# Performance work log

Measured on AMD Instinct MI355X. Metric: run time of the kernel, lower is better.

## Reference

```python
import jax, jax.numpy as jnp
import numpy as np

B, S, V, E, HL = 64, 30, 5000, 300, 256
TWOH = 2 * HL
KB, MAPD, MEMD, MLP, NCLS = 512, 512, 512, 1024, 32
L, T, NMOD, NOPS = 8, 9, 9, 6
IH, IW, CIN = 15, 10, 512 + 128


def setup_inputs():
    key = jax.random.key(0)
    ks = iter(jax.random.split(key, 64))
    g = lambda shape, s=0.05: jax.random.normal(next(ks), shape, jnp.float32) * s
    inp = {}
    inp['image'] = g((B, CIN, IH, IW), 1.0)
    inp['ques'] = jax.random.randint(next(ks), (B, S), 0, V)
    ql = jnp.sort(jax.random.randint(next(ks), (B,), 1, S + 1))[::-1]
    inp['q_len'] = ql.at[0].set(S)
    inp['embed_W'] = g((V, E))
    for d in ('f', 'b'):
        inp['lstm_Wi_' + d] = g((E, 4 * HL))
        inp['lstm_Wh_' + d] = g((HL, 4 * HL))
        inp['lstm_b_' + d] = jnp.zeros((4 * HL,), jnp.float32)
    inp['W1'] = g((T, TWOH, TWOH))
    inp['b_1'] = jnp.zeros((TWOH,), jnp.float32)
    inp['W2_w'] = g((2 * TWOH, TWOH)); inp['W2_b'] = jnp.zeros((TWOH,), jnp.float32)
    inp['W3'] = g((TWOH,))
    inp['c_0'] = g((TWOH,), 1.0)
    inp['Wmod'] = g((TWOH, NMOD))
    inp['ic1_w'] = g((KB, CIN)); inp['ic1_b'] = g((KB,), 1.0)
    inp['ic2_w'] = g((KB, KB)); inp['ic2_b'] = g((KB,), 1.0)
    inp['i2m_w'] = g((MAPD, KB)); inp['i2m_b'] = g((MAPD,), 1.0)
    inp['t2m_w'] = g((TWOH, MAPD)); inp['t2m_b'] = jnp.zeros((MAPD,), jnp.float32)
    inp['cell3_ow'] = g((4, NOPS), 1.0)
    inp['cell3_cw'] = g((4, MAPD)); inp['cell3_cb'] = jnp.zeros((4,), jnp.float32)
    inp['cell4_ow'] = g((2, NOPS), 1.0)
    inp['cell4_cw'] = g((2, MAPD)); inp['cell4_cb'] = jnp.zeros((2,), jnp.float32)
    inp['ans_ow'] = g((2, NOPS), 1.0)
    inp['ans_W'] = g((2, 2 * MAPD, MEMD)); inp['ans_b'] = jnp.zeros((2, MEMD), jnp.float32)
    inp['out1_w'] = g((TWOH + MEMD, MLP)); inp['out1_b'] = jnp.zeros((MLP,), jnp.float32)
    inp['out2_w'] = g((MLP, NCLS)); inp['out2_b'] = jnp.zeros((NCLS,), jnp.float32)
    return inp


def _conv1x1(x, w, b):
    return jnp.einsum('bchw,oc->bohw', x, w) + b[None, :, None, None]


def _lstm_dir(xW, Wh, mask, reverse):
    # xW: [S,B,4H], mask: [S,B,1] ; torch LSTM gate order i,f,g,o
    Bn, Hn = xW.shape[1], Wh.shape[0]
    def step(carry, inp):
        h, c = carry
        xw, m = inp
        z = xw + h @ Wh
        i, f, gg, o = jnp.split(z, 4, axis=-1)
        cn = jax.nn.sigmoid(f) * c + jax.nn.sigmoid(i) * jnp.tanh(gg)
        hn = jax.nn.sigmoid(o) * jnp.tanh(cn)
        return (jnp.where(m, hn, h), jnp.where(m, cn, c)), jnp.where(m, hn, 0.0)
    init = (jnp.zeros((Bn, Hn), xW.dtype), jnp.zeros((Bn, Hn), xW.dtype))
    (hF, _), outs = jax.lax.scan(step, init, (xW, mask), reverse=reverse)
    return hF, outs


def _mix3(ow, x, a, t):
    # soft op mixing (DARTS-style) for 3-input cells: x [B,D,H,W], a [B,H,W], t [B,D]
    w = jax.nn.softmax(ow)
    a4 = a[:, None]; t4 = t[:, :, None, None]
    ops = (x * t4, x + t4, x * a4, x * t4 * a4, x, a4 * t4)
    return jax.nn.elu(sum(w[k] * ops[k] for k in range(NOPS)))


def _mix4(ow, x, a1, a2, t):
    w = jax.nn.softmax(ow)
    a14 = a1[:, None]; a24 = a2[:, None]; t4 = t[:, :, None, None]
    ops = (x * t4, x + t4, x * a14, x * a24, x * a14 * a24, x * t4 * (a14 + a24))
    return jax.nn.elu(sum(w[k] * ops[k] for k in range(NOPS)))


def _forward(image, ques, q_len, embed_W, lstm_Wi_f, lstm_Wh_f, lstm_b_f, lstm_Wi_b, lstm_Wh_b, lstm_b_b, W1, b_1, W2_w, W2_b, W3, c_0, Wmod, ic1_w, ic1_b, ic2_w, ic2_b, i2m_w, i2m_b, t2m_w, t2m_b, cell3_ow, cell3_cw, cell3_cb, cell4_ow, cell4_cw, cell4_cb, ans_ow, ans_W, ans_b, out1_w, out1_b, out2_w, out2_b):
    # img_conv (1x1 conv -> ELU -> 1x1 conv)
    x = jax.nn.elu(_conv1x1(image, ic1_w, ic1_b))
    x = _conv1x1(x, ic2_w, ic2_b)
    Bn, _, Hh, Ww = x.shape
    Sn = ques.shape[1]
    # bi-LSTM over the (packed, i.e. masked) question
    emb = embed_W[ques]                                   # [B,S,E]
    mask = (jnp.arange(Sn)[None, :] < q_len[:, None])     # [B,S]
    mT = mask.T[:, :, None].astype(x.dtype) > 0           # [S,B,1] bool
    xWf = (emb @ lstm_Wi_f + lstm_b_f).transpose(1, 0, 2)
    xWb = (emb @ lstm_Wi_b + lstm_b_b).transpose(1, 0, 2)
    hF, oF = _lstm_dir(xWf, lstm_Wh_f, mT, False)
    hB, oB = _lstm_dir(xWb, lstm_Wh_b, mT, True)
    lstm_out = jnp.concatenate([oF, oB], -1).transpose(1, 0, 2)  # [B,S,2H], zero at pads
    q = jnp.concatenate([hF, hB], -1)                            # [B,2H]
    img_map = _conv1x1(x, i2m_w, i2m_b)                          # [B,MAP,H,W]
    stack = jnp.zeros((Bn, Hh, Ww, L), x.dtype)
    p = jnp.zeros((Bn, L), x.dtype).at[:, 0].set(1.0)
    mem = jnp.zeros((Bn, MEMD), x.dtype)
    c_prev = jnp.tile(c_0[None], (Bn, 1))
    e0 = jnp.zeros((L,), x.dtype).at[0].set(1.0)
    imp_loss = jnp.float32(0.0)
    read = lambda st, pp: jnp.einsum('bhwl,bl->bhw', st, pp)
    dec = lambda pp: jnp.concatenate([pp[:, 1:], jnp.zeros_like(pp[:, :1])], 1) + pp * e0
    for t in range(T):
        u = jnp.concatenate([q @ W1[t] + b_1, c_prev], 1) @ W2_w + W2_b  # [B,2H]
        wl = u @ Wmod                                                     # [B,9]
        ls = jax.nn.log_softmax(wl, axis=1)
        imp_loss = imp_loss - jnp.sum(jnp.exp(ls) * ls)
        w = jnp.exp(ls)
        attn = jax.nn.softmax(jnp.einsum('bsh,h->bs', lstm_out * u[:, None, :], W3), axis=1)
        c = jnp.einsum('bs,bsh->bh', attn, lstm_out)
        c_prev = c
        tmap = c @ t2m_w + t2m_b
        stacks, ps = [], []
        a_top = read(stack, p)     # attention at stack top
        # modules 0-3: overwrite at current pointer (pointer shift is commented out in source)
        for m in range(4):
            out = jnp.einsum('bdhw,d->bhw', _mix3(cell3_ow[m], img_map, a_top, tmap), cell3_cw[m]) + cell3_cb[m]
            pb = p[:, None, None, :]
            stacks.append(stack * (1.0 - pb) + out[..., None] * pb)
            ps.append(p)
        # modules 4-5: pop one (soft pointer decrement), then write
        p_dec = dec(p)
        a2 = read(stack, p_dec)
        for m in range(2):
            out = jnp.einsum('bdhw,d->bhw', _mix4(cell4_ow[m], img_map, a_top, a2, tmap), cell4_cw[m]) + cell4_cb[m]
            pb = p_dec[:, None, None, :]
            stacks.append(stack * (1.0 - pb) + out[..., None] * pb)
            ps.append(p_dec)
        # modules 6-7: answer cells -> memory update, stack untouched
        pooled6 = jnp.mean(_mix3(ans_ow[0], img_map, a_top, tmap), axis=(2, 3))
        mem6 = jnp.concatenate([pooled6, tmap], 1) @ ans_W[0] + ans_b[0]
        stacks.append(stack); ps.append(p)
        pooled7 = jnp.mean(_mix4(ans_ow[1], img_map, a_top, a2, tmap), axis=(2, 3))
        mem7 = jnp.concatenate([pooled7, tmap], 1) @ ans_W[1] + ans_b[1]
        stacks.append(stack); ps.append(p_dec)
        # module 8: NoOp
        stacks.append(stack); ps.append(p)
        # soft mixing over modules (the scatter-heavy part)
        stack = jnp.einsum('bm,bmhwl->bhwl', w, jnp.stack(stacks, 1))
        p = jnp.einsum('bm,bml->bl', w, jnp.stack(ps, 1))
        mem = w[:, 6:7] * mem6 + w[:, 7:8] * mem7 + (1.0 - w[:, 6:7] - w[:, 7:8]) * mem
    h1 = jax.nn.elu(jnp.concatenate([q, mem], 1) @ out1_w + out1_b)
    logits = h1 @ out2_w + out2_b
    return logits, imp_loss


def reference(image, ques, q_len, embed_W, lstm_Wi_f, lstm_Wh_f, lstm_b_f, lstm_Wi_b, lstm_Wh_b, lstm_b_b, W1, b_1, W2_w, W2_b, W3, c_0, Wmod, ic1_w, ic1_b, ic2_w, ic2_b, i2m_w, i2m_b, t2m_w, t2m_b, cell3_ow, cell3_cw, cell3_cb, cell4_ow, cell4_cw, cell4_cb, ans_ow, ans_W, ans_b, out1_w, out1_b, out2_w, out2_b):
    return _forward(image, ques, q_len, embed_W, lstm_Wi_f, lstm_Wh_f, lstm_b_f, lstm_Wi_b, lstm_Wh_b, lstm_b_b, W1, b_1, W2_w, W2_b, W3, c_0, Wmod, ic1_w, ic1_b, ic2_w, ic2_b, i2m_w, i2m_b, t2m_w, t2m_b, cell3_ow, cell3_cw, cell3_cb, cell4_ow, cell4_cw, cell4_cb, ans_ow, ans_W, ans_b, out1_w, out1_b, out2_w, out2_b)
```

## Files before the change

kernel.cpp:

```cpp
#include <hip/hip_runtime.h>
#include <hip/hip_fp16.h>
#include <math.h>

#define DEV __device__ __forceinline__

DEV float fexp(float x){ return __expf(x); }
DEV float elu_(float x){ return x > 0.f ? x : fexp(x) - 1.f; }
DEV float sigm_(float x){ return 1.f/(1.f + fexp(-x)); }
DEV float tanh_(float x){ float e = fexp(2.f*x); return 1.f - 2.f/(e + 1.f); }
DEV unsigned bf16r(float x){ unsigned u = __float_as_uint(x);
  return (u + 0x7fffu + ((u>>16)&1u)) >> 16; }
DEV float blo(unsigned u){ return __uint_as_float(u << 16); }
DEV float bhi(unsigned u){ return __uint_as_float(u & 0xffff0000u); }
DEV float bl(unsigned short u){ return __uint_as_float(((unsigned)u) << 16); }

using frag  = __attribute__((ext_vector_type(8))) short;
using fragh = __attribute__((ext_vector_type(8))) _Float16;
using f32x4 = __attribute__((ext_vector_type(4))) float;

DEV uint4 cload16w(const void* p){
  uint4 r;
  asm volatile("global_load_dwordx4 %0, %1, off sc0 sc1\n\ts_waitcnt vmcnt(0)"
               : "=v"(r) : "v"(p) : "memory");
  return r;
}
DEV uint4 cload16nw(const void* p){
  uint4 r;
  asm volatile("global_load_dwordx4 %0, %1, off sc0 sc1"
               : "=v"(r) : "v"(p) : "memory");
  return r;
}

DEV void d_packB(const float* __restrict__ W, short* __restrict__ Bp,
                 int KC, int Ng, int Ksrc, int N, int trans, int idx)
{
  if (idx >= KC*Ng*64) return;
  int lane = idx & 63;
  int g    = (idx >> 6) % Ng;
  int kc   = idx / (64*Ng);
  int n = g*16 + (lane & 15);
  int kb = kc*32 + ((lane >> 4) << 3);
  unsigned o[4];
#pragma unroll
  for (int jj = 0; jj < 4; ++jj) {
    int k0 = kb + 2*jj;
    float v0 = (k0   < Ksrc) ? (trans ? W[(size_t)n*Ksrc + k0]   : W[(size_t)(k0)*N + n])   : 0.f;
    float v1 = (k0+1 < Ksrc) ? (trans ? W[(size_t)n*Ksrc + k0+1] : W[(size_t)(k0+1)*N + n]) : 0.f;
    o[jj] = bf16r(v0) | (bf16r(v1) << 16);
  }
  *(uint4*)(Bp + (size_t)idx*8) = make_uint4(o[0], o[1], o[2], o[3]);
}

DEV void d_packImg(const float* __restrict__ image, short* __restrict__ Ap, int idx)
{
  int lane = idx & 63;
  int kc   = (idx >> 6) % 20;
  int mt   = idx / 1280;
  int row = mt*16 + (lane & 15);
  int b = row / 150, p = row % 150;
  int cb = kc*32 + ((lane >> 4) << 3);
  unsigned o[4];
#pragma unroll
  for (int jj = 0; jj < 4; ++jj) {
    float v0 = image[((size_t)b*640 + cb + 2*jj    )*150 + p];
    float v1 = image[((size_t)b*640 + cb + 2*jj + 1)*150 + p];
    o[jj] = bf16r(v0) | (bf16r(v1) << 16);
  }
  *(uint4*)(Ap + (size_t)idx*8) = make_uint4(o[0], o[1], o[2], o[3]);
}

DEV void d_packEmb(const float* __restrict__ embedW, const int* __restrict__ ques,
                   short* __restrict__ Ap, int idx)
{
  int lane = idx & 63;
  int kc   = (idx >> 6) % 10;
  int mt   = idx / 640;
  int row = mt*16 + (lane & 15);
  int q = ques[row];
  int kb = kc*32 + ((lane >> 4) << 3);
  unsigned o[4];
#pragma unroll
  for (int jj = 0; jj < 4; ++jj) {
    int k0 = kb + 2*jj;
    float v0 = (k0   < 300) ? embedW[(size_t)q*300 + k0]   : 0.f;
    float v1 = (k0+1 < 300) ? embedW[(size_t)q*300 + k0+1] : 0.f;
    o[jj] = bf16r(v0) | (bf16r(v1) << 16);
  }
  *(uint4*)(Ap + (size_t)idx*8) = make_uint4(o[0], o[1], o[2], o[3]);
}

__global__ __launch_bounds__(256)
void megapack_k(const float* __restrict__ c0, const float* __restrict__ c3ow,
                const float* __restrict__ c4ow, const float* __restrict__ aow,
                float* __restrict__ stack, float* __restrict__ pvecA,
                float* __restrict__ mem, float* __restrict__ cprev,
                float* __restrict__ swb, float* __restrict__ pl,
                const float* __restrict__ Whf, const float* __restrict__ Whb,
                unsigned* __restrict__ whT,
                float* __restrict__ hbufz, int* __restrict__ flagz,
                const float* __restrict__ ic1w, short* __restrict__ w1p,
                const float* __restrict__ ic2w, short* __restrict__ w2mp,
                const float* __restrict__ i2mw, short* __restrict__ w3mp,
                const float* __restrict__ Wif, short* __restrict__ wifp,
                const float* __restrict__ Wib, short* __restrict__ wibp,
                const float* __restrict__ image, short* __restrict__ imgP,
                const float* __restrict__ embedW, const int* __restrict__ ques,
                short* __restrict__ embp,
                const float* __restrict__ t2mw, unsigned* __restrict__ t2pp,
                const float* __restrict__ W2w, unsigned short* __restrict__ w2bp,
                const float* __restrict__ ansW, unsigned short* __restrict__ answp)
{
  const int bx = blockIdx.x, tid = threadIdx.x;
  if (bx < 320) {
    int idx = bx*256 + tid;
    int stride = 320*256;
    for (int i = idx; i < 64*150*8; i += stride) stack[i] = 0.f;
    for (int i = idx; i < 64*8;    i += stride) pvecA[i] = ((i & 7) == 0) ? 1.f : 0.f;
    for (int i = idx; i < 64*512;  i += stride) mem[i] = 0.f;
    for (int i = idx; i < 64*512;  i += stride) cprev[i] = c0[i & 511];
    for (int i = idx; i < 9*2*64*512; i += stride) pl[i] = 0.f;
    for (int i = idx; i < 32768;   i += stride) hbufz[i] = 0.f;
    if (idx < 256) flagz[idx] = 0;
    if (idx < 8) {
      const float* ow = (idx < 4) ? (c3ow + idx*6)
                      : (idx < 6) ? (c4ow + (idx-4)*6)
                                  : (aow  + (idx-6)*6);
      float mx = ow[0];
      for (int m = 1; m < 6; ++m) mx = fmaxf(mx, ow[m]);
      float e[6]; float s = 0.f;
      for (int m = 0; m < 6; ++m) { e[m] = fexp(ow[m]-mx); s += e[m]; }
      for (int m = 0; m < 6; ++m) swb[idx*6+m] = e[m]/s;
    }
  } else if (bx < 1344) {
    int idx = (bx-320)*256 + tid;
    int dd  = idx >> 17;
    int rem = idx & 131071;
    int kp  = rem >> 10;
    int zc  = rem & 1023;
    const float* Wh = dd ? Whb : Whf;
    __half2 hv = __floats2half2_rn(Wh[(size_t)(2*kp)*1024 + zc],
                                   Wh[(size_t)(2*kp+1)*1024 + zc]);
    whT[((size_t)dd << 17) + (zc << 7) + kp] = *(unsigned*)&hv;
  } else if (bx < 1504) {
    d_packB(ic1w, w1p, 20, 32, 640, 512, 1, (bx-1344)*256 + tid);
  } else if (bx < 1632) {
    d_packB(ic2w, w2mp, 16, 32, 512, 512, 1, (bx-1504)*256 + tid);
  } else if (bx < 1760) {
    d_packB(i2mw, w3mp, 16, 32, 512, 512, 1, (bx-1632)*256 + tid);
  } else if (bx < 1920) {
    d_packB(Wif, wifp, 10, 64, 300, 1024, 0, (bx-1760)*256 + tid);
  } else if (bx < 2080) {
    d_packB(Wib, wibp, 10, 64, 300, 1024, 0, (bx-1920)*256 + tid);
  } else if (bx < 5080) {
    d_packImg(image, imgP, (bx-2080)*256 + tid);
  } else if (bx < 5380) {
    d_packEmb(embedW, ques, embp, (bx-5080)*256 + tid);
  } else if (bx < 5892) {
    int idx = (bx-5380)*256 + tid;
    int k = idx >> 8, c = idx & 255;
    t2pp[idx] = bf16r(t2mw[(size_t)k*512 + c]) | (bf16r(t2mw[(size_t)k*512 + 256 + c]) << 16);
  } else if (bx < 7940) {
    int i = (bx-5892)*256 + tid;
    w2bp[i] = (unsigned short)bf16r(W2w[i]);
  } else {
    int i = (bx-7940)*256 + tid;
    answp[i] = (unsigned short)bf16r(ansW[i]);
  }
}

__global__ __launch_bounds__(256)
void gemmM_k(const short* __restrict__ ApA, const short* __restrict__ ApB,
             const short* __restrict__ BpA, const short* __restrict__ BpB,
             const float* __restrict__ biasA, const float* __restrict__ biasB,
             void* __restrict__ CoutA, void* __restrict__ CoutB,
             int KC, int Ng, int N, int mode, int act, int KCout)
{
  __shared__ float lds[4][16][68];
  const int z = blockIdx.z;
  const short* Ap = z ? ApB : ApA;
  const short* Bp = z ? BpB : BpA;
  const float* bias = z ? biasB : biasA;
  void* Cout = z ? CoutB : CoutA;
  const int tid = threadIdx.x, lane = tid & 63, w = tid >> 6;
  const int mt = blockIdx.y*4 + w;
  const int ncol0 = blockIdx.x*64;
  const short* Abase = Ap + (((size_t)mt*KC) << 9) + lane*8;
  const short* Bbase = Bp + (((size_t)blockIdx.x*4) << 9) + lane*8;
  f32x4 acc0 = {0.f,0.f,0.f,0.f}, acc1 = acc0, acc2 = acc0, acc3 = acc0;
#pragma unroll 2
  for (int kc = 0; kc < KC; ++kc) {
    frag a = *(const frag*)(Abase + ((size_t)kc << 9));
    const short* bk = Bbase + (((size_t)kc*Ng) << 9);
    frag b0 = *(const frag*)(bk);
    frag b1 = *(const frag*)(bk + 512);
    frag b2 = *(const frag*)(bk + 1024);
    frag b3 = *(const frag*)(bk + 1536);
    acc0 = __builtin_amdgcn_mfma_f32_16x16x32_bf16(a, b0, acc0, 0, 0, 0);
    acc1 = __builtin_amdgcn_mfma_f32_16x16x32_bf16(a, b1, acc1, 0, 0, 0);
    acc2 = __builtin_amdgcn_mfma_f32_16x16x32_bf16(a, b2, acc2, 0, 0, 0);
    acc3 = __builtin_amdgcn_mfma_f32_16x16x32_bf16(a, b3, acc3, 0, 0, 0);
  }
  {
    int colb = lane & 15, rowb = (lane >> 4)*4;
#pragma unroll
    for (int r = 0; r < 4; ++r) {
      lds[w][rowb+r][ 0+colb] = acc0[r];
      lds[w][rowb+r][16+colb] = acc1[r];
      lds[w][rowb+r][32+colb] = acc2[r];
      lds[w][rowb+r][48+colb] = acc3[r];
    }
  }
  __syncthreads();
  if (mode == 0) {
    float* C = (float*)Cout;
    int mloc = lane >> 2, q4 = lane & 3;
    size_t rowoff = (size_t)(mt*16 + mloc)*N + ncol0 + q4*16;
#pragma unroll
    for (int i = 0; i < 4; ++i) {
      float4 v = *(float4*)&lds[w][mloc][q4*16 + i*4];
      const float* bp = bias + ncol0 + q4*16 + i*4;
      v.x += bp[0]; v.y += bp[1]; v.z += bp[2]; v.w += bp[3];
      if (act) { v.x = elu_(v.x); v.y = elu_(v.y); v.z = elu_(v.z); v.w = elu_(v.w); }
      *(float4*)&C[rowoff + i*4] = v;
    }
  } else if (mode == 1) {
    short* C = (short*)Cout;
    int m = lane & 15, qb = (lane >> 4)*8;
#pragma unroll
    for (int h = 0; h < 2; ++h) {
      int nl = h*32 + qb;
      unsigned o[4];
#pragma unroll
      for (int jj = 0; jj < 4; ++jj) {
        float v0 = lds[w][m][nl + 2*jj]     + bias[ncol0 + nl + 2*jj];
        float v1 = lds[w][m][nl + 2*jj + 1] + bias[ncol0 + nl + 2*jj + 1];
        if (act) { v0 = elu_(v0); v1 = elu_(v1); }
        o[jj] = bf16r(v0) | (bf16r(v1) << 16);
      }
      *(uint4*)(C + (((size_t)mt*KCout + (ncol0 >> 5) + h) << 9) + lane*8)
          = make_uint4(o[0], o[1], o[2], o[3]);
    }
  } else {
    unsigned short* C = (unsigned short*)Cout;
    int row = lane >> 2, cb = (lane & 3)*16;
#pragma unroll
    for (int h = 0; h < 2; ++h) {
      unsigned o[4];
#pragma unroll
      for (int jj = 0; jj < 4; ++jj) {
        float v0 = lds[w][row][cb + h*8 + 2*jj]     + bias[ncol0 + cb + h*8 + 2*jj];
        float v1 = lds[w][row][cb + h*8 + 2*jj + 1] + bias[ncol0 + cb + h*8 + 2*jj + 1];
        if (act) { v0 = elu_(v0); v1 = elu_(v1); }
        o[jj] = bf16r(v0) | (bf16r(v1) << 16);
      }
      *(uint4*)&C[(size_t)(mt*16 + row)*N + ncol0 + cb + h*8]
          = make_uint4(o[0], o[1], o[2], o[3]);
    }
  }
}

__global__ __launch_bounds__(512)
void gemm64b_k(const float* __restrict__ A1, long zA1, int K1log,
               const float* __restrict__ A2, int K2,
               const float* __restrict__ B, long zB,
               const float* __restrict__ bias, int zbias,
               float* __restrict__ C, long zC, int N, int act)
{
  const int K1 = 1 << K1log;
  const int Kt = K1 + K2;
  __shared__ __align__(16) float As[8][1024];
  __shared__ float part[8][8][64];
  const int tid = threadIdx.x;
  const int z = blockIdx.z;
  const int r0 = blockIdx.y*8;
  {
    const float* a1 = A1 + (size_t)z*zA1;
    const int nf4 = (8*K1) >> 2;
    for (int e4 = tid; e4 < nf4; e4 += 512) {
      int r = e4 >> (K1log-2);
      int k4 = (e4 & ((K1>>2)-1)) << 2;
      *(float4*)&As[r][k4] = *(const float4*)&a1[(size_t)(r0+r)*K1 + k4];
    }
    if (K2 > 0) {
      for (int e4 = tid; e4 < 1024; e4 += 512) {
        int r = e4 >> 7;
        int k4 = (e4 & 127) << 2;
        *(float4*)&As[r][K1+k4] = *(const float4*)&A2[(size_t)(r0+r)*512 + k4];
      }
    }
  }
  __syncthreads();
  const int lane = tid & 63, w = tid >> 6;
  const int n = blockIdx.x*64 + lane;
  const bool nv = n < N;
  const int kseg = Kt >> 3;
  const int k0 = w*kseg;
  const float* Bp = B + (size_t)z*zB + (size_t)k0*N + (nv ? n : 0);
  float acc[8] = {0,0,0,0,0,0,0,0};
#pragma unroll 8
  for (int kk = 0; kk < kseg; ++kk) {
    float bv = nv ? Bp[(size_t)kk*N] : 0.f;
    int k = k0 + kk;
#pragma unroll
    for (int r = 0; r < 8; ++r) acc[r] += As[r][k]*bv;
  }
#pragma unroll
  for (int r = 0; r < 8; ++r) part[w][r][lane] = acc[r];
  __syncthreads();
  {
    int r = tid >> 6, c = tid & 63;
    int nn = blockIdx.x*64 + c;
    if (nn < N) {
      float s = 0.f;
#pragma unroll
      for (int w2 = 0; w2 < 8; ++w2) s += part[w2][r][c];
      s += bias ? bias[(size_t)z*zbias + nn] : 0.f;
      if (act == 1) s = elu_(s);
      C[(size_t)z*zC + (size_t)(r0+r)*N + nn] = s;
    }
  }
}

__global__ __launch_bounds__(256)
void lstmM_k(const float* __restrict__ xWf, const float* __restrict__ xWb,
             const unsigned* __restrict__ whT, const int* __restrict__ qlen,
             unsigned long long* __restrict__ hbuf, int* __restrict__ flags,
             float* __restrict__ lstm_out, float* __restrict__ qout)
{
  const int bx = blockIdx.x;
  const int d = bx & 1, g = (bx >> 1) & 3, n = bx >> 3;
  const int tid = threadIdx.x, lane = tid & 63, w = tid >> 6;
  const int q = lane >> 4, cl = lane & 15;
  __shared__ __align__(16) unsigned short Wl[65536];

#pragma unroll 4
  for (int rb = 0; rb < 32; ++rb) {
    int lcrow = rb*8 + (tid >> 5);
    int gt = lcrow >> 6, c = lcrow & 63;
    int zc = gt*256 + n*64 + c;
    uint4 v = *(const uint4*)(whT + (((size_t)d*1024 + zc) << 7) + ((tid & 31) << 2));
    int byteoff = (lcrow << 9) + ((((tid & 31) << 4)) ^ ((lcrow & 7) << 4));
    *(uint4*)((char*)Wl + byteoff) = v;
  }

  const float* xW = d ? xWb : xWf;
  const int b   = g*16 + cl;
  const int c4  = w*16 + q*4;
  const int hc4 = n*64 + c4;
  const int len = qlen[b];
  float cst[4] = {0.f,0.f,0.f,0.f}, hst[4] = {0.f,0.f,0.f,0.f};
  int* flg = flags + ((d*4 + g) << 2);
  const int bofs = (cl & 7) << 4;
  __syncthreads();

  for (int ss = 0; ss < 30; ++ss) {
    const int s = d ? (29 - ss) : ss;
    const float* xr = xW + (size_t)b*30720 + (size_t)s*1024 + hc4;
    f32x4 xwv[4];
#pragma unroll
    for (int gt = 0; gt < 4; ++gt) xwv[gt] = *(const f32x4*)(xr + gt*256);

    if (ss > 0) {
      for (;;) {
        uint4 f4 = cload16w(flg);
        if ((int)f4.x >= ss && (int)f4.y >= ss &&
            (int)f4.z >= ss && (int)f4.w >= ss) break;
      }
      __builtin_amdgcn_sched_barrier(0);
    }
    const char* hbr = (const char*)(hbuf + ((size_t)(((ss & 1)*2 + d)*4 + g) << 9))
                    + (cl << 9) + (q << 4);
    union { uint4 u; fragh f; } hv[8];
#pragma unroll
    for (int ks = 0; ks < 8; ++ks) hv[ks].u = cload16nw(hbr + (ks << 6));
    asm volatile("s_waitcnt vmcnt(0)" ::: "memory");
    __builtin_amdgcn_sched_barrier(0);

    f32x4 acc0 = {0.f,0.f,0.f,0.f}, acc1 = acc0, acc2 = acc0, acc3 = acc0;
#pragma unroll
    for (int ks = 0; ks < 8; ++ks) {
      const int kb = ((ks << 6) + (q << 4)) ^ bofs;
      const char* wb = (const char*)Wl + ((w*16 + cl) << 9) + kb;
      fragh a0 = *(const fragh*)(wb);
      fragh a1 = *(const fragh*)(wb + (64 << 9));
      fragh a2 = *(const fragh*)(wb + (128 << 9));
      fragh a3 = *(const fragh*)(wb + (192 << 9));
      acc0 = __builtin_amdgcn_mfma_f32_16x16x32_f16(a0, hv[ks].f, acc0, 0, 0, 0);
      acc1 = __builtin_amdgcn_mfma_f32_16x16x32_f16(a1, hv[ks].f, acc1, 0, 0, 0);
      acc2 = __builtin_amdgcn_mfma_f32_16x16x32_f16(a2, hv[ks].f, acc2, 0, 0, 0);
      acc3 = __builtin_amdgcn_mfma_f32_16x16x32_f16(a3, hv[ks].f, acc3, 0, 0, 0);
    }
    const bool m = s < len;
    f32x4 lo4;
    float hvv[4];
#pragma unroll
    for (int r = 0; r < 4; ++r) {
      float iv = acc0[r] + xwv[0][r];
      float fv = acc1[r] + xwv[1][r];
      float gv = acc2[r] + xwv[2][r];
      float o_ = acc3[r] + xwv[3][r];
      float cn = sigm_(fv)*cst[r] + sigm_(iv)*tanh_(gv);
      float hn = sigm_(o_)*tanh_(cn);
      float hk = m ? hn : hst[r];
      cst[r] = m ? cn : cst[r];
      hst[r] = hk;
      hvv[r] = hk;
      lo4[r] = m ? hn : 0.f;
    }
    unsigned long long* hbw = hbuf + ((size_t)((((ss & 1) ^ 1)*2 + d)*4 + g) << 9);
    union { unsigned long long u; __half2 h2[2]; } hp;
    hp.h2[0] = __floats2half2_rn(hvv[0], hvv[1]);
    hp.h2[1] = __floats2half2_rn(hvv[2], hvv[3]);
    __hip_atomic_store(hbw + cl*64 + (hc4 >> 2), hp.u,
                       __ATOMIC_RELAXED, __HIP_MEMORY_SCOPE_AGENT);
    *(f32x4*)(lstm_out + (((size_t)b*30 + s) << 9) + (d << 8) + hc4) = lo4;
    asm volatile("s_waitcnt vmcnt(0)" ::: "memory");
    __syncthreads();
    if (tid == 0)
      __hip_atomic_store(&flg[n], ss + 1, __ATOMIC_RELAXED, __HIP_MEMORY_SCOPE_AGENT);
  }
  *(f32x4*)(qout + ((size_t)b << 9) + (d << 8) + hc4) =
      f32x4{hst[0], hst[1], hst[2], hst[3]};
}

__global__ __launch_bounds__(1024)
void kcattn3_k(const float* __restrict__ u, const float* __restrict__ Wmod,
               const float* __restrict__ lstm_out, const float* __restrict__ W3,
               const unsigned* __restrict__ t2pp, const float* __restrict__ t2mb,
               float* __restrict__ woutAll, float* __restrict__ imp_part,
               float* __restrict__ cout, float* __restrict__ tmapv, int t)
{
  int b = blockIdx.x;
  int tid = threadIdx.x;
  int lane = tid & 63, wave = tid >> 6;
  __shared__ float ush[512];
  __shared__ float sC[512];
  __shared__ float cpart[512];
  __shared__ float tpart[4][512];
  __shared__ float wl[9];
  __shared__ float sc[32], at[32];
  if (tid < 512) ush[tid] = u[b*512 + tid];
  __syncthreads();
  for (int s = wave; s < 30; s += 16) {
    float acc = 0.f;
    const float* lo = lstm_out + ((size_t)b*30 + s)*512;
#pragma unroll
    for (int h = lane; h < 512; h += 64) acc += lo[h]*ush[h]*W3[h];
#pragma unroll
    for (int off = 32; off; off >>= 1) acc += __shfl_down(acc, off);
    if (lane == 0) sc[s] = acc;
  }
  if (wave < 9) {
    float acc = 0.f;
#pragma unroll
    for (int k = lane; k < 512; k += 64) acc += ush[k]*Wmod[k*9+wave];
#pragma unroll
    for (int off = 32; off; off >>= 1) acc += __shfl_down(acc, off);
    if (lane == 0) wl[wave] = acc;
  }
  __syncthreads();
  if (tid == 0) {
    float mx = wl[0];
    for (int m = 1; m < 9; ++m) mx = fmaxf(mx, wl[m]);
    float s = 0.f;
    for (int m = 0; m < 9; ++m) s += fexp(wl[m]-mx);
    float ls = logf(s);
    float ent = 0.f;
    for (int m = 0; m < 9; ++m) {
      float l = wl[m]-mx-ls;
      float w = fexp(l);
      woutAll[t*576 + b*9 + m] = w;
      ent -= w*l;
    }
    imp_part[t*64+b] = ent;
  }
  if (wave == 1) {
    float v = (lane < 30) ? sc[lane] : -3.4e38f;
    float mx = v;
#pragma unroll
    for (int off = 32; off; off >>= 1) mx = fmaxf(mx, __shfl_xor(mx, off));
    float e = (lane < 30) ? fexp(v-mx) : 0.f;
    float ssum = e;
#pragma unroll
    for (int off = 32; off; off >>= 1) ssum += __shfl_xor(ssum, off);
    if (lane < 30) at[lane] = e/ssum;
  }
  __syncthreads();
  {
    int h = tid & 511, seg = tid >> 9;
    float acc = 0.f;
    int s0 = seg ? 15 : 0, s1 = seg ? 30 : 15;
    for (int s = s0; s < s1; ++s) acc += at[s]*lstm_out[((size_t)b*30 + s)*512 + h];
    if (seg) cpart[h] = acc;
    __syncthreads();
    if (!seg) {
      float tot = acc + cpart[h];
      cout[b*512+h] = tot;
      sC[h] = tot;
    }
  }
  __syncthreads();
  {
    int c2 = tid & 255, ks = tid >> 8;
    float a0 = 0.f, a1 = 0.f;
    const unsigned* tp = t2pp + c2;
#pragma unroll 8
    for (int k = ks*128; k < ks*128 + 128; ++k) {
      float cv = sC[k];
      unsigned wv2 = tp[(size_t)k*256];
      a0 += cv*blo(wv2);
      a1 += cv*bhi(wv2);
    }
    tpart[ks][c2]       = a0;
    tpart[ks][256 + c2] = a1;
  }
  __syncthreads();
  if (tid < 512) {
    float v = tpart[0][tid] + tpart[1][tid] + tpart[2][tid] + tpart[3][tid];
    tmapv[b*512 + tid] = v + t2mb[tid];
  }
}

__global__ __launch_bounds__(256)
void modu_k(const unsigned short* __restrict__ imapB, const float* __restrict__ tmapv,
            float* __restrict__ stack, const float* __restrict__ pvecIn,
            float* __restrict__ pvecOut,
            const float* __restrict__ swb, const float* __restrict__ c3w,
            const float* __restrict__ c3b, const float* __restrict__ c4w,
            const float* __restrict__ c4b, const float* __restrict__ wmod,
            float* __restrict__ plt,
            const float* __restrict__ tmp1n, const float* __restrict__ cprevB,
            const unsigned short* __restrict__ w2bp, const float* __restrict__ W2b,
            float* __restrict__ ubuf, int do_u)
{
  __shared__ union {
    struct { float sT[512]; float pv[8], pd[8], wm[9]; float wpart[4][2][512]; } m;
    struct { __align__(16) float As[8][1024]; float part[4][8][64]; } u;
  } sm;
  int pb = blockIdx.y;
  int lane = threadIdx.x & 63, wave = threadIdx.x >> 6;
  if (pb == 19) {
    if (!do_u) return;
    const int x = blockIdx.x;
    const int r0 = (x >> 3) * 8, nc0 = (x & 7) * 64;
    for (int e4 = threadIdx.x; e4 < 2048; e4 += 256) {
      int r = e4 >> 8;
      int k4 = (e4 & 255) << 2;
      float4 v = (k4 < 512)
          ? *(const float4*)&tmp1n [(size_t)(r0+r)*512 + k4]
          : *(const float4*)&cprevB[(size_t)(r0+r)*512 + (k4 - 512)];
      *(float4*)&sm.u.As[r][k4] = v;
    }
    __syncthreads();
    const int k0 = wave * 256;
    const unsigned short* Bp = w2bp + (size_t)k0*512 + nc0 + lane;
    float acc[8] = {0,0,0,0,0,0,0,0};
#pragma unroll 4
    for (int kk = 0; kk < 256; ++kk) {
      float bv = bl(Bp[(size_t)kk*512]);
#pragma unroll
      for (int r = 0; r < 8; ++r) acc[r] += sm.u.As[r][k0+kk] * bv;
    }
#pragma unroll
    for (int r = 0; r < 8; ++r) sm.u.part[wave][r][lane] = acc[r];
    __syncthreads();
    {
      int r = threadIdx.x >> 6, c = lane;
#pragma unroll
      for (int p2 = 0; p2 < 2; ++p2) {
        int rr = r + p2*4;
        float s2 = sm.u.part[0][rr][c] + sm.u.part[1][rr][c]
                 + sm.u.part[2][rr][c] + sm.u.part[3][rr][c];
        ubuf[(size_t)(r0 + rr)*512 + nc0 + c] = s2 + W2b[nc0 + c];
      }
    }
    return;
  }
  int b = blockIdx.x;
  for (int j = threadIdx.x; j < 512; j += 256) sm.m.sT[j] = tmapv[b*512 + j];
  if (threadIdx.x < 8) sm.m.pv[threadIdx.x] = pvecIn[b*8+threadIdx.x];
  if (threadIdx.x >= 64 && threadIdx.x < 73) sm.m.wm[threadIdx.x-64] = wmod[b*9 + threadIdx.x-64];
  __syncthreads();
  if (threadIdx.x < 8) {
    int l = threadIdx.x;
    sm.m.pd[l] = (l < 7 ? sm.m.pv[l+1] : 0.f) + (l == 0 ? sm.m.pv[0] : 0.f);
  }
  __syncthreads();
  if (pb == 0 && threadIdx.x < 8) {
    int l = threadIdx.x;
    float WP = sm.m.wm[0]+sm.m.wm[1]+sm.m.wm[2]+sm.m.wm[3] + sm.m.wm[6] + sm.m.wm[8];
    float WD = sm.m.wm[4]+sm.m.wm[5] + sm.m.wm[7];
    pvecOut[b*8+l] = WP*sm.m.pv[l] + WD*sm.m.pd[l];
  }

  float W[8][6];
#pragma unroll
  for (int m = 0; m < 8; ++m)
#pragma unroll
    for (int i = 0; i < 6; ++i) W[m][i] = swb[m*6+i];
  float W03 = sm.m.wm[0]+sm.m.wm[1]+sm.m.wm[2]+sm.m.wm[3];
  float W45 = sm.m.wm[4]+sm.m.wm[5];

  float acc6[8], acc7[8];
#pragma unroll
  for (int i = 0; i < 8; ++i) { acc6[i] = 0.f; acc7[i] = 0.f; }

  for (int pi = 0; pi < 2; ++pi) {
    int p = pb*8 + wave*2 + pi;
    if (p < 150) {
      const float* st = stack + ((size_t)b*150 + p)*8;
      float a = 0.f, av2 = 0.f;
#pragma unroll
      for (int l = 0; l < 8; ++l) { float v = st[l]; a += v*sm.m.pv[l]; av2 += v*sm.m.pd[l]; }
      float part[6] = {0,0,0,0,0,0};
#pragma unroll 2
      for (int i = 0; i < 8; ++i) {
        int d = i*64 + lane;
        float x = bl(imapB[((size_t)b*150 + p)*512 + d]);
        float t = sm.m.sT[d];
#pragma unroll
        for (int m = 0; m < 4; ++m) {
          float c1 = W[m][0]*t + W[m][1] + W[m][4] + (W[m][2] + W[m][3]*t)*a;
          float c0 = W[m][1]*t + W[m][5]*t*a;
          part[m] += elu_(c1*x + c0) * c3w[m*512+d];
        }
#pragma unroll
        for (int m = 0; m < 2; ++m) {
          float c1 = W[4+m][0]*t + W[4+m][1] + W[4+m][2]*a + W[4+m][3]*av2
                   + W[4+m][4]*a*av2 + W[4+m][5]*t*(a+av2);
          part[4+m] += elu_(c1*x + W[4+m][1]*t) * c4w[m*512+d];
        }
        float c16 = W[6][0]*t + W[6][1] + W[6][4] + (W[6][2] + W[6][3]*t)*a;
        float c06 = W[6][1]*t + W[6][5]*t*a;
        acc6[i] += elu_(c16*x + c06);
        float c17 = W[7][0]*t + W[7][1] + W[7][2]*a + W[7][3]*av2
                  + W[7][4]*a*av2 + W[7][5]*t*(a+av2);
        acc7[i] += elu_(c17*x + W[7][1]*t);
      }
#pragma unroll
      for (int m = 0; m < 6; ++m) {
#pragma unroll
        for (int off = 32; off; off >>= 1) part[m] += __shfl_down(part[m], off);
        part[m] = __shfl(part[m], 0);
      }
      float r3  = sm.m.wm[0]*(part[0]+c3b[0]) + sm.m.wm[1]*(part[1]+c3b[1])
                + sm.m.wm[2]*(part[2]+c3b[2]) + sm.m.wm[3]*(part[3]+c3b[3]);
      float r45 = sm.m.wm[4]*(part[4]+c4b[0]) + sm.m.wm[5]*(part[5]+c4b[1]);
      if (lane < 8) {
        int l = lane;
        size_t idx = ((size_t)b*150 + p)*8 + l;
        stack[idx] = stack[idx]*(1.f - W03*sm.m.pv[l] - W45*sm.m.pd[l])
                   + sm.m.pv[l]*r3 + sm.m.pd[l]*r45;
      }
    }
  }
#pragma unroll
  for (int i = 0; i < 8; ++i) {
    sm.m.wpart[wave][0][i*64+lane] = acc6[i];
    sm.m.wpart[wave][1][i*64+lane] = acc7[i];
  }
  __syncthreads();
  for (int e = threadIdx.x; e < 1024; e += 256) {
    int which = e >> 9, d = e & 511;
    float s = sm.m.wpart[0][which][d] + sm.m.wpart[1][which][d]
            + sm.m.wpart[2][which][d] + sm.m.wpart[3][which][d];
    atomicAdd(&plt[(size_t)which*32768 + b*512 + d], s * (1.f/150.f));
  }
}

__global__ __launch_bounds__(512)
void ansall_k(const float* __restrict__ plt, const float* __restrict__ tmapv,
              const unsigned short* __restrict__ answp, const float* __restrict__ ansb,
              float* __restrict__ m67o)
{
  const int z = blockIdx.z;
  const int t = z >> 1, zz = z & 1;
  __shared__ __align__(16) float As[8][1024];
  __shared__ float part[8][8][64];
  const int tid = threadIdx.x;
  const int r0 = blockIdx.y*8;
  const int nc0 = blockIdx.x*64;
  const int lane = tid & 63, w = tid >> 6;

  for (int e4 = tid; e4 < 1024; e4 += 512) {
    int r = e4 >> 7, k4 = (e4 & 127) << 2;
    *(float4*)&As[r][k4]     = *(const float4*)&plt[(size_t)z*32768 + (size_t)(r0+r)*512 + k4];
    *(float4*)&As[r][512+k4] = *(const float4*)&tmapv[(size_t)t*32768 + (size_t)(r0+r)*512 + k4];
  }
  __syncthreads();
  {
    const unsigned short* Bp = answp + (size_t)zz*524288
                             + (size_t)(w*128)*512 + nc0 + lane;
    float acc[8] = {0,0,0,0,0,0,0,0};
    int k0 = w*128;
#pragma unroll 8
    for (int kk = 0; kk < 128; ++kk) {
      float bv = bl(Bp[(size_t)kk*512]);
#pragma unroll
      for (int r = 0; r < 8; ++r) acc[r] += As[r][k0+kk]*bv;
    }
#pragma unroll
    for (int r = 0; r < 8; ++r) part[w][r][lane] = acc[r];
  }
  __syncthreads();
  {
    int r = tid >> 6, c = tid & 63;
    float s = 0.f;
#pragma unroll
    for (int w2 = 0; w2 < 8; ++w2) s += part[w2][r][c];
    m67o[(size_t)z*32768 + (size_t)(r0+r)*512 + nc0 + c] = s + ansb[zz*512 + nc0 + c];
  }
}

__global__ __launch_bounds__(512)
void memfin_k(const float* __restrict__ woutAll, const float* __restrict__ m67t,
              float* __restrict__ memb)
{
  int b = blockIdx.x;
  int tid = threadIdx.x;
  __shared__ float w6s[9], w7s[9], coef[9];
  if (tid < 9)       w6s[tid] = woutAll[tid*576 + b*9 + 6];
  else if (tid < 18) w7s[tid-9] = woutAll[(tid-9)*576 + b*9 + 7];
  __syncthreads();
  if (tid == 0) {
    float c = 1.f;
    for (int t = 8; t >= 0; --t) { coef[t] = c; c *= (1.f - w6s[t] - w7s[t]); }
  }
  __syncthreads();
  float acc = 0.f;
#pragma unroll
  for (int t = 0; t < 9; ++t) {
    float m6 = m67t[(((size_t)t*2 + 0)*64 + b)*512 + tid];
    float m7 = m67t[(((size_t)t*2 + 1)*64 + b)*512 + tid];
    acc += coef[t]*(w6s[t]*m6 + w7s[t]*m7);
  }
  memb[b*512 + tid] = acc;
}

__global__ __launch_bounds__(256)
void imp_k(const float* __restrict__ part, float* __restrict__ out)
{
  int lane = threadIdx.x & 63, wave = threadIdx.x >> 6;
  float acc = 0.f;
  for (int i = threadIdx.x; i < 576; i += 256) acc += part[i];
#pragma unroll
  for (int off = 32; off; off >>= 1) acc += __shfl_down(acc, off);
  __shared__ float red[4];
  if (lane == 0) red[wave] = acc;
  __syncthreads();
  if (threadIdx.x == 0) out[0] = red[0]+red[1]+red[2]+red[3];
}

extern "C" void kernel_launch(void* const* d_in, const int* in_sizes, int n_in,
                              void* d_out, int out_size, void* d_ws, size_t ws_size,
                              hipStream_t stream)
{
  (void)in_sizes; (void)n_in; (void)out_size; (void)ws_size;
  const float* image = (const float*)d_in[0];
  const int*   ques  = (const int*)d_in[1];
  const int*   qlen  = (const int*)d_in[2];
  const float* embedW= (const float*)d_in[3];
  const float* Wi_f  = (const float*)d_in[4];
  const float* Wh_f  = (const float*)d_in[5];
  const float* b_f   = (const float*)d_in[6];
  const float* Wi_b  = (const float*)d_in[7];
  const float* Wh_b  = (const float*)d_in[8];
  const float* b_b   = (const float*)d_in[9];
  const float* W1    = (const float*)d_in[10];
  const float* b1    = (const float*)d_in[11];
  const float* W2w   = (const float*)d_in[12];
  const float* W2b   = (const float*)d_in[13];
  const float* W3    = (const float*)d_in[14];
  const float* c0    = (const float*)d_in[15];
  const float* Wmod  = (const float*)d_in[16];
  const float* ic1w  = (const float*)d_in[17];
  const float* ic1b  = (const float*)d_in[18];
  const float* ic2w  = (const float*)d_in[19];
  const float* ic2b  = (const float*)d_in[20];
  const float* i2mw  = (const float*)d_in[21];
  const float* i2mb  = (const float*)d_in[22];
  const float* t2mw  = (const float*)d_in[23];
  const float* t2mb  = (const float*)d_in[24];
  const float* c3ow  = (const float*)d_in[25];
  const float* c3cw  = (const float*)d_in[26];
  const float* c3cb  = (const float*)d_in[27];
  const float* c4ow  = (const float*)d_in[28];
  const float* c4cw  = (const float*)d_in[29];
  const float* c4cb  = (const float*)d_in[30];
  const float* aow   = (const float*)d_in[31];
  const float* ansW  = (const float*)d_in[32];
  const float* ansb  = (const float*)d_in[33];
  const float* o1w   = (const float*)d_in[34];
  const float* o1b   = (const float*)d_in[35];
  const float* o2w   = (const float*)d_in[36];
  const float* o2b   = (const float*)d_in[37];
  float* out = (float*)d_out;
  float* ws  = (float*)d_ws;

  size_t off = 0;
  auto alloc = [&](size_t n){ float* p = ws + off; off += n; return p; };
  short* imgP  = (short*)alloc(600ull*20*64*8/2);
  short* X1p   = (short*)alloc(600ull*16*64*8/2);
  short* X2p   = (short*)alloc(600ull*16*64*8/2);
  short* w1p   = (short*)alloc(20*32*64*8/2);
  short* w2mp  = (short*)alloc(16*32*64*8/2);
  short* w3mp  = (short*)alloc(16*32*64*8/2);
  short* wifp  = (short*)alloc(10*64*64*8/2);
  short* wibp  = (short*)alloc(10*64*64*8/2);
  short* embp  = (short*)alloc(120ull*10*64*8/2);
  unsigned short* imapB = (unsigned short*)alloc(9600ull*512/2);
  unsigned* t2pp = (unsigned*)alloc(512*256);
  unsigned short* w2bp  = (unsigned short*)alloc(524288/2);
  unsigned short* answp = (unsigned short*)alloc(1048576/2);
  float* xWfb  = alloc(64ull*30*1024);
  float* xWbb  = alloc(64ull*30*1024);
  float* lout  = alloc(64ull*30*512);
  float* qbuf  = alloc(64*512);
  float* stck  = alloc(64*150*8);
  float* pvecA = alloc(64*8);
  float* pvecB = alloc(64*8);
  float* memb  = alloc(64*512);
  float* cprev = alloc(64*512);
  float* tmp1a = alloc(9ull*64*512);
  float* ubuf  = alloc(64*512);
  float* wmwA  = alloc(9*64*9);
  float* impp  = alloc(9*64);
  float* swb   = alloc(48);
  float* pl    = alloc(9ull*2*64*512);
  float* m67t  = alloc(9ull*2*64*512);
  float* tmapv = alloc(9ull*64*512);
  float* h1b   = alloc(64*1024);
  unsigned* whT = (unsigned*)alloc(2ull*1024*128);
  float* hbufW  = alloc(32768);
  int*   flagsI = (int*)alloc(256);

  megapack_k<<<12036, 256, 0, stream>>>(
      c0, c3ow, c4ow, aow, stck, pvecA, memb, cprev, swb, pl,
      Wh_f, Wh_b, whT, hbufW, flagsI,
      ic1w, w1p, ic2w, w2mp, i2mw, w3mp, Wi_f, wifp, Wi_b, wibp,
      image, imgP, embedW, ques, embp, t2mw, t2pp,
      W2w, w2bp, ansW, answp);

  gemmM_k<<<dim3(8,150,1), 256, 0, stream>>>(imgP, imgP, w1p, w1p, ic1b, ic1b,
                                             X1p, X1p, 20, 32, 512, 1, 1, 16);
  gemmM_k<<<dim3(8,150,1), 256, 0, stream>>>(X1p, X1p, w2mp, w2mp, ic2b, ic2b,
                                             X2p, X2p, 16, 32, 512, 1, 0, 16);
  gemmM_k<<<dim3(8,150,1), 256, 0, stream>>>(X2p, X2p, w3mp, w3mp, i2mb, i2mb,
                                             imapB, imapB, 16, 32, 512, 2, 0, 0);
  gemmM_k<<<dim3(16,30,2), 256, 0, stream>>>(embp, embp, wifp, wibp, b_f, b_b,
                                             xWfb, xWbb, 10, 64, 1024, 0, 0, 0);

  lstmM_k<<<32, 256, 0, stream>>>(xWfb, xWbb, whT, qlen,
                                  (unsigned long long*)hbufW, flagsI, lout, qbuf);

  gemm64b_k<<<dim3(8,8,9), 512, 0, stream>>>(
      qbuf, 0, 9, (const float*)nullptr, 0,
      W1, 262144, b1, 0, tmp1a, 32768, 512, 0);
  gemm64b_k<<<dim3(8,8,1), 512, 0, stream>>>(
      tmp1a, 0, 9, cprev, 512, W2w, 0, W2b, 0, ubuf, 0, 512, 0);

  for (int t = 0; t < 9; ++t) {
    float* pvIn  = (t & 1) ? pvecB : pvecA;
    float* pvOut = (t & 1) ? pvecA : pvecB;
    kcattn3_k<<<64, 1024, 0, stream>>>(ubuf, Wmod, lout, W3, t2pp, t2mb,
                                       wmwA, impp, cprev,
                                       tmapv + (size_t)t*32768, t);
    modu_k<<<dim3(64,20), 256, 0, stream>>>(
        imapB, tmapv + (size_t)t*32768, stck, pvIn, pvOut, swb,
        c3cw, c3cb, c4cw, c4cb,
        wmwA + (size_t)t*576, pl + (size_t)t*65536,
        tmp1a + (size_t)(t < 8 ? t+1 : 0)*32768, cprev, w2bp, W2b, ubuf,
        (t < 8) ? 1 : 0);
  }

  ansall_k<<<dim3(8,8,18), 512, 0, stream>>>(pl, tmapv, answp, ansb, m67t);

  memfin_k<<<64, 512, 0, stream>>>(wmwA, m67t, memb);
  gemm64b_k<<<dim3(16,8,1), 512, 0, stream>>>(
      qbuf, 0, 9, memb, 512, o1w, 0, o1b, 0, h1b, 0, 1024, 1);
  gemm64b_k<<<dim3(1,8,1), 512, 0, stream>>>(
      h1b, 0, 10, (const float*)nullptr, 0, o2w, 0, o2b, 0, out, 0, 32, 0);
  imp_k<<<1, 256, 0, stream>>>(impp, out + 2048);
}
```

Measured before the change: 833.6 us.

## Co-schedule first image conv GEMM inside the LSTM kernel launch

Merges the first 1x1 image conv GEMM (ic1, with ELU and bf16 packing) into the same launch as the latency-bound 32-block LSTM recurrence. Extra blocks beyond the first 32 compute conv tiles, so those GEMM blocks fill otherwise idle CUs while the LSTM blocks spin on flags. The xW GEMM is moved ahead so the fused kernel has its inputs. The risk is that the LSTM blocks rely on inter-block flag polling. If GEMM blocks delay their scheduling or compete with them for memory bandwidth, the recurrence could slow down. Sharing LDS through a union may also affect occupancy.

```diff
diff --git a/kernel.cpp b/kernel.cpp
--- a/kernel.cpp
+++ b/kernel.cpp
@@ -322,16 +322,72 @@
 }
 
 __global__ __launch_bounds__(256)
-void lstmM_k(const float* __restrict__ xWf, const float* __restrict__ xWb,
-             const unsigned* __restrict__ whT, const int* __restrict__ qlen,
-             unsigned long long* __restrict__ hbuf, int* __restrict__ flags,
-             float* __restrict__ lstm_out, float* __restrict__ qout)
-{
+void lstmc1_k(const float* __restrict__ xWf, const float* __restrict__ xWb,
+              const unsigned* __restrict__ whT, const int* __restrict__ qlen,
+              unsigned long long* __restrict__ hbuf, int* __restrict__ flags,
+              float* __restrict__ lstm_out, float* __restrict__ qout,
+              const short* __restrict__ c1Ap, const short* __restrict__ c1Bp,
+              const float* __restrict__ c1bias, short* __restrict__ c1out)
+{
+  const int tid = threadIdx.x, lane = tid & 63, w = tid >> 6;
+  __shared__ union {
+    unsigned short Wl[65536];
+    float lds[4][16][68];
+  } sm;
+
+  if (blockIdx.x >= 32) {
+    const int bx2 = (int)blockIdx.x - 32;
+    const int mt = (bx2 >> 3)*4 + w;
+    const int ncol0 = (bx2 & 7)*64;
+    const short* Abase = c1Ap + (((size_t)mt*20) << 9) + lane*8;
+    const short* Bbase = c1Bp + (((size_t)(bx2 & 7)*4) << 9) + lane*8;
+    f32x4 acc0 = {0.f,0.f,0.f,0.f}, acc1 = acc0, acc2 = acc0, acc3 = acc0;
+#pragma unroll 2
+    for (int kc = 0; kc < 20; ++kc) {
+      frag a = *(const frag*)(Abase + ((size_t)kc << 9));
+      const short* bk = Bbase + (((size_t)kc*32) << 9);
+      frag b0 = *(const frag*)(bk);
+      frag b1 = *(const frag*)(bk + 512);
+      frag b2 = *(const frag*)(bk + 1024);
+      frag b3 = *(const frag*)(bk + 1536);
+      acc0 = __builtin_amdgcn_mfma_f32_16x16x32_bf16(a, b0, acc0, 0, 0, 0);
+      acc1 = __builtin_amdgcn_mfma_f32_16x16x32_bf16(a, b1, acc1, 0, 0, 0);
+      acc2 = __builtin_amdgcn_mfma_f32_16x16x32_bf16(a, b2, acc2, 0, 0, 0);
+      acc3 = __builtin_amdgcn_mfma_f32_16x16x32_bf16(a, b3, acc3, 0, 0, 0);
+    }
+    {
+      int colb = lane & 15, rowb = (lane >> 4)*4;
+#pragma unroll
+      for (int r = 0; r < 4; ++r) {
+        sm.lds[w][rowb+r][ 0+colb] = acc0[r];
+        sm.lds[w][rowb+r][16+colb] = acc1[r];
+        sm.lds[w][rowb+r][32+colb] = acc2[r];
+        sm.lds[w][rowb+r][48+colb] = acc3[r];
+      }
+    }
+    __syncthreads();
+    {
+      int m = lane & 15, qb = (lane >> 4)*8;
+#pragma unroll
+      for (int h = 0; h < 2; ++h) {
+        int nl = h*32 + qb;
+        unsigned o[4];
+#pragma unroll
+        for (int jj = 0; jj < 4; ++jj) {
+          float v0 = elu_(sm.lds[w][m][nl + 2*jj]     + c1bias[ncol0 + nl + 2*jj]);
+          float v1 = elu_(sm.lds[w][m][nl + 2*jj + 1] + c1bias[ncol0 + nl + 2*jj + 1]);
+          o[jj] = bf16r(v0) | (bf16r(v1) << 16);
+        }
+        *(uint4*)(c1out + (((size_t)mt*16 + (ncol0 >> 5) + h) << 9) + lane*8)
+            = make_uint4(o[0], o[1], o[2], o[3]);
+      }
+    }
+    return;
+  }
+
   const int bx = blockIdx.x;
   const int d = bx & 1, g = (bx >> 1) & 3, n = bx >> 3;
-  const int tid = threadIdx.x, lane = tid & 63, w = tid >> 6;
   const int q = lane >> 4, cl = lane & 15;
-  __shared__ __align__(16) unsigned short Wl[65536];
 
 #pragma unroll 4
   for (int rb = 0; rb < 32; ++rb) {
@@ -340,7 +396,7 @@
     int zc = gt*256 + n*64 + c;
     uint4 v = *(const uint4*)(whT + (((size_t)d*1024 + zc) << 7) + ((tid & 31) << 2));
     int byteoff = (lcrow << 9) + ((((tid & 31) << 4)) ^ ((lcrow & 7) << 4));
-    *(uint4*)((char*)Wl + byteoff) = v;
+    *(uint4*)((char*)sm.Wl + byteoff) = v;
   }
 
   const float* xW = d ? xWb : xWf;
@@ -380,7 +436,7 @@
 #pragma unroll
     for (int ks = 0; ks < 8; ++ks) {
       const int kb = ((ks << 6) + (q << 4)) ^ bofs;
-      const char* wb = (const char*)Wl + ((w*16 + cl) << 9) + kb;
+      const char* wb = (const char*)sm.Wl + ((w*16 + cl) << 9) + kb;
       fragh a0 = *(const fragh*)(wb);
       fragh a1 = *(const fragh*)(wb + (64 << 9));
       fragh a2 = *(const fragh*)(wb + (128 << 9));
@@ -841,17 +897,18 @@
       image, imgP, embedW, ques, embp, t2mw, t2pp,
       W2w, w2bp, ansW, answp);
 
-  gemmM_k<<<dim3(8,150,1), 256, 0, stream>>>(imgP, imgP, w1p, w1p, ic1b, ic1b,
-                                             X1p, X1p, 20, 32, 512, 1, 1, 16);
+  gemmM_k<<<dim3(16,30,2), 256, 0, stream>>>(embp, embp, wifp, wibp, b_f, b_b,
+                                             xWfb, xWbb, 10, 64, 1024, 0, 0, 0);
+
+  lstmc1_k<<<1232, 256, 0, stream>>>(xWfb, xWbb, whT, qlen,
+                                     (unsigned long long*)hbufW, flagsI,
+                                     lout, qbuf,
+                                     imgP, w1p, ic1b, X1p);
+
   gemmM_k<<<dim3(8,150,1), 256, 0, stream>>>(X1p, X1p, w2mp, w2mp, ic2b, ic2b,
                                              X2p, X2p, 16, 32, 512, 1, 0, 16);
   gemmM_k<<<dim3(8,150,1), 256, 0, stream>>>(X2p, X2p, w3mp, w3mp, i2mb, i2mb,
                                              imapB, imapB, 16, 32, 512, 2, 0, 0);
-  gemmM_k<<<dim3(16,30,2), 256, 0, stream>>>(embp, embp, wifp, wibp, b_f, b_b,
-                                             xWfb, xWbb, 10, 64, 1024, 0, 0, 0);
-
-  lstmM_k<<<32, 256, 0, stream>>>(xWfb, xWbb, whT, qlen,
-                                  (unsigned long long*)hbufW, flagsI, lout, qbuf);
 
   gemm64b_k<<<dim3(8,8,9), 512, 0, stream>>>(
       qbuf, 0, 9, (const float*)nullptr, 0,
```

Measured after the change: 811.0 us. 2.7% less time.
